# Optimization experiments

Measured on AMD Instinct MI355X. Metric: run time of the kernel, lower is better.

The kernel has to match this reference:

```python
import jax, jax.numpy as jnp
import numpy as np

N = 10000       # nodes
E = 160000      # edges
B = 100         # graphs
F_NODE = 32
F_EDGE = 16
H0, H1, H2, H3, H4, H5 = 32, 64, 128, 256, 128, 64
EPS = 1e-5


def setup_inputs() -> dict:
    key = jax.random.key(0)
    ks = jax.random.split(key, 32)

    def rn(k, shape):
        fan_in = shape[0] if len(shape) > 1 else shape[0]
        return jax.random.normal(k, shape, jnp.float32) / np.float32(np.sqrt(fan_in))

    inp = {}
    inp["x"] = jax.random.normal(ks[0], (N, F_NODE), jnp.float32)
    inp["edge_index"] = jax.random.randint(ks[1], (2, E), 0, N)
    inp["edge_attr"] = jax.random.normal(ks[2], (E, F_EDGE), jnp.float32)
    inp["batch"] = jnp.sort(jax.random.randint(ks[3], (N,), 0, B))
    # EdgeMLP: F_EDGE -> 128 -> 64 -> F_NODE*H0
    inp["We1"] = rn(ks[4], (F_EDGE, 128)); inp["be1"] = jnp.zeros((128,), jnp.float32)
    inp["We2"] = rn(ks[5], (128, 64));     inp["be2"] = jnp.zeros((64,), jnp.float32)
    inp["We3"] = rn(ks[6], (64, F_NODE * H0)); inp["be3"] = jnp.zeros((F_NODE * H0,), jnp.float32)
    # NNConv root linear + bias
    inp["Wroot"] = rn(ks[7], (F_NODE, H0)); inp["bc1"] = jnp.zeros((H0,), jnp.float32)
    # GATConv 1 (H0 -> H1, heads=1)
    inp["Wg1"] = rn(ks[8], (H0, H1)); inp["as1"] = rn(ks[9], (H1,)); inp["ad1"] = rn(ks[10], (H1,)); inp["bg1"] = jnp.zeros((H1,), jnp.float32)
    # GATConv 2 (H1 -> H2, heads=1)
    inp["Wg2"] = rn(ks[11], (H1, H2)); inp["as2"] = rn(ks[12], (H2,)); inp["ad2"] = rn(ks[13], (H2,)); inp["bg2"] = jnp.zeros((H2,), jnp.float32)
    # FC head
    inp["Wf1"] = rn(ks[14], (H2, H3)); inp["bf1"] = jnp.zeros((H3,), jnp.float32)
    inp["Wf2"] = rn(ks[15], (H3, H4)); inp["bf2"] = jnp.zeros((H4,), jnp.float32)
    inp["Wf3"] = rn(ks[16], (H4, H5)); inp["bf3"] = jnp.zeros((H5,), jnp.float32)
    return inp


def _bn(h):  # training-mode BatchNorm1d, affine = identity (default init)
    m = h.mean(axis=0)
    v = h.var(axis=0)
    return (h - m) * jax.lax.rsqrt(v + EPS)


def _seg_softmax(e, seg, n):
    m = jax.ops.segment_max(e, seg, num_segments=n)
    ex = jnp.exp(e - m[seg])
    s = jax.ops.segment_sum(ex, seg, num_segments=n)
    return ex / (s[seg] + 1e-16)


def _gat(x, src, dst, W, a_src, a_dst, b):
    n = x.shape[0]
    h = x @ W                                     # [N, F_out]
    loop = jnp.arange(n)                          # PyG add_self_loops=True
    s = jnp.concatenate([src, loop])
    d = jnp.concatenate([dst, loop])
    sc_s = h @ a_src                              # [N]
    sc_d = h @ a_dst
    e = jax.nn.leaky_relu(sc_s[s] + sc_d[d], negative_slope=0.2)
    alpha = _seg_softmax(e, d, n)                 # segment softmax over in-edges
    out = jax.ops.segment_sum(alpha[:, None] * h[s], d, num_segments=n)
    return out + b


def reference(x, edge_index, edge_attr, batch,
              We1, be1, We2, be2, We3, be3, Wroot, bc1,
              Wg1, as1, ad1, bg1, Wg2, as2, ad2, bg2,
              Wf1, bf1, Wf2, bf2, Wf3, bf3):
    src, dst = edge_index[0], edge_index[1]

    # --- NNConv: per-edge weight matrices from EdgeMLP ---
    t = jax.nn.relu(edge_attr @ We1 + be1)
    t = jax.nn.relu(t @ We2 + be2)
    theta = (t @ We3 + be3).reshape(E, F_NODE, H0)        # [E, F_in, F_out]
    msg = jnp.einsum('ef,efo->eo', x[src], theta)          # gather-matmul
    agg = jax.ops.segment_sum(msg, dst, num_segments=N)    # scatter-add (aggr='add')
    h = agg + x @ Wroot + bc1
    h = jax.nn.relu(_bn(h))

    # --- GATConv x2 ---
    h = jax.nn.relu(_bn(_gat(h, src, dst, Wg1, as1, ad1, bg1)))
    h = jax.nn.relu(_bn(_gat(h, src, dst, Wg2, as2, ad2, bg2)))

    # --- global mean pool ---
    sums = jax.ops.segment_sum(h, batch, num_segments=B)
    cnts = jax.ops.segment_sum(jnp.ones((N,), h.dtype), batch, num_segments=B)
    g = sums / jnp.maximum(cnts, 1.0)[:, None]             # [B, H2]

    # --- MLP head (dropout=Identity in eval/reference) ---
    g = jax.nn.relu(_bn(g @ Wf1 + bf1))
    g = jax.nn.relu(_bn(g @ Wf2 + bf2))
    return g @ Wf3 + bf3                                   # [B, H5]
```

## Files before the change

### kernel.cpp

```cpp
#include <hip/hip_runtime.h>

#define NN 10000
#define NE 160000
#define NGB 100

typedef __attribute__((ext_vector_type(8))) short s8v;
typedef __attribute__((ext_vector_type(4))) float f4v;
typedef __attribute__((ext_vector_type(2))) _Float16 h2v;
typedef __attribute__((ext_vector_type(8))) _Float16 h8v;

static __device__ __forceinline__ float lrelu(float v){ return v > 0.f ? v : 0.2f*v; }
static __device__ __forceinline__ unsigned short f2bf(float f){
  unsigned u = __float_as_uint(f);
  u += 0x7fffu + ((u >> 16) & 1u);
  return (unsigned short)(u >> 16);
}
static __device__ __forceinline__ float bf2f(unsigned short h){
  return __uint_as_float(((unsigned)h) << 16);
}
static __device__ __forceinline__ unsigned pkh(float a, float b){
  auto h = __builtin_amdgcn_cvt_pkrtz(a, b);
  return __builtin_bit_cast(unsigned, h);
}
static __device__ __forceinline__ unsigned short f2h(float f){
  _Float16 h = (_Float16)f;
  return __builtin_bit_cast(unsigned short, h);
}
static __device__ __forceinline__ float h2f(unsigned short u){
  return (float)__builtin_bit_cast(_Float16, u);
}

__global__ __launch_bounds__(256) void k_deg_bounds(const int* __restrict__ src, const int* __restrict__ dst,
                                                    const int* __restrict__ batch,
                                                    int* deg_src, int* deg_dst, int* starts){
  int i = blockIdx.x*256 + threadIdx.x;
  if (i < NE){ atomicAdd(&deg_src[src[i]],1); atomicAdd(&deg_dst[dst[i]],1); }
  if (i <= NN){
    int cur  = (i==NN) ? NGB : batch[i];
    int prev = (i==0)  ? -1  : batch[i-1];
    for (int b=prev+1; b<=cur; b++) if (b<=NGB) starts[b]=i;
  }
}

__global__ __launch_bounds__(1024) void k_scan(const int* __restrict__ deg_src, const int* __restrict__ deg_dst,
                                               int* rp_src, int* rp_dst){
  const int* deg = (blockIdx.x==0) ? deg_src : deg_dst;
  int* rp = (blockIdx.x==0) ? rp_src : rp_dst;
  __shared__ int part[1024];
  int tid = threadIdx.x;
  const int per = (NN + 1023)/1024;
  int base = tid*per;
  int s = 0;
  for (int i=0;i<per;i++){ int idx=base+i; if (idx<NN) s += deg[idx]; }
  part[tid]=s; __syncthreads();
  for (int off=1; off<1024; off<<=1){
    int v = part[tid];
    int add = (tid>=off) ? part[tid-off] : 0;
    __syncthreads();
    part[tid] = v + add;
    __syncthreads();
  }
  int run = (tid==0) ? 0 : part[tid-1];
  for (int i=0;i<per;i++){ int idx=base+i; if (idx<NN){ rp[idx]=run; run += deg[idx]; } }
  if (tid==1023) rp[NN] = part[1023];
}

__global__ __launch_bounds__(256) void k_fill(const int* __restrict__ src, const int* __restrict__ dst,
                       const int* __restrict__ rp_src, const int* __restrict__ rp_dst,
                       int* fill_src, int* fill_dst, int* pos_src, int* dstp, int* srcd, int* dstd){
  int i = blockIdx.x*256 + threadIdx.x;
  if (i < NE){
    int s=src[i], d=dst[i];
    int p=rp_src[s]+atomicAdd(&fill_src[s],1); pos_src[i]=p; dstp[p]=d;
    int q=rp_dst[d]+atomicAdd(&fill_dst[d],1); srcd[q]=s; dstd[q]=d;
  }
}

__global__ __launch_bounds__(256) void k_packall(const float* __restrict__ We1, const float* __restrict__ be1,
    const float* __restrict__ We2, const float* __restrict__ We3,
    unsigned short* __restrict__ W1p, unsigned short* __restrict__ W2p,
    unsigned short* __restrict__ W3h, unsigned short* __restrict__ W3l){
  int tid = threadIdx.x;
  if (blockIdx.x == 32){
    for (int idx=tid; idx<512; idx+=256){
      int j=idx>>6, l=idx&63, col=l&15, g=l>>4;
      int out = j*16+col;
      #pragma unroll
      for (int jj=0;jj<8;jj++){
        int k = g*8+jj;
        float v = (k<16) ? We1[k*128+out] : (k==16 ? be1[out] : 0.f);
        W1p[idx*8+jj] = f2bf(v);
      }
    }
    for (int idx=tid; idx<1024; idx+=256){
      int ft=idx>>6, l=idx&63, col=l&15, g=l>>4;
      int t=ft>>2, jo=ft&3;
      int out = jo*16+col;
      #pragma unroll
      for (int jj=0;jj<8;jj++){
        int k = t*32+g*8+jj;
        W2p[idx*8+jj] = f2bf(We2[k*64+out]);
      }
    }
  } else {
    int idx = blockIdx.x*256 + tid;
    int jt = idx>>6, l = idx&63;
    int j = jt*16 + (l&15);
    int f0 = (l>>4)*8;
    int k = j>>5, o = j&31;
    #pragma unroll
    for (int jj=0;jj<8;jj++){
      float v = We3[(size_t)k*1024 + (size_t)(f0+jj)*32 + o];
      unsigned short h = f2bf(v);
      float r = v - bf2f(h);
      W3h[(size_t)idx*8+jj] = h;
      W3l[(size_t)idx*8+jj] = f2bf(r);
    }
  }
}

__global__ __launch_bounds__(256) void k_edge_mlp2(const float* __restrict__ ea,
    const unsigned short* __restrict__ W1p, const unsigned short* __restrict__ W2p,
    const float* __restrict__ be2, const int* __restrict__ pos_src, unsigned* __restrict__ t2b){
  __shared__ unsigned short st1[4*2048];
  int tid=threadIdx.x, wave=tid>>6, lane=tid&63;
  int c = lane&15, g = lane>>4;
  s8v w1f[8], w2f[16];
  #pragma unroll
  for (int j=0;j<8;j++)  w1f[j] = *(const s8v*)(W1p + (size_t)(j*64+lane)*8);
  #pragma unroll
  for (int q=0;q<16;q++) w2f[q] = *(const s8v*)(W2p + (size_t)(q*64+lane)*8);
  float be2v[16];
  #pragma unroll
  for (int jo=0;jo<4;jo++)
    #pragma unroll
    for (int r=0;r<4;r++) be2v[jo*4+r] = be2[jo*16+g*4+r];
  char* myld = (char*)(st1 + wave*2048);
  const f4v fzero = {0.f,0.f,0.f,0.f};

  for (int base = blockIdx.x*64; base < NE; base += gridDim.x*64){
    int e0 = base + wave*16;
    s8v eaf = {0,0,0,0,0,0,0,0};
    if (g < 2){
      const float* p = ea + (size_t)(e0+c)*16 + g*8;
      float4 a = *(const float4*)p;
      float4 b = *(const float4*)(p+4);
      eaf[0]=(short)f2bf(a.x); eaf[1]=(short)f2bf(a.y); eaf[2]=(short)f2bf(a.z); eaf[3]=(short)f2bf(a.w);
      eaf[4]=(short)f2bf(b.x); eaf[5]=(short)f2bf(b.y); eaf[6]=(short)f2bf(b.z); eaf[7]=(short)f2bf(b.w);
    } else if (g == 2){
      eaf[0] = (short)0x3f80;
    }
    f4v acc1[8];
    #pragma unroll
    for (int j=0;j<8;j++)
      acc1[j] = __builtin_amdgcn_mfma_f32_16x16x32_bf16(w1f[j], eaf, fzero, 0, 0, 0);
    #pragma unroll
    for (int j=0;j<8;j++){
      unsigned lo = (unsigned)f2bf(fmaxf(acc1[j][0],0.f)) | ((unsigned)f2bf(fmaxf(acc1[j][1],0.f))<<16);
      unsigned hi = (unsigned)f2bf(fmaxf(acc1[j][2],0.f)) | ((unsigned)f2bf(fmaxf(acc1[j][3],0.f))<<16);
      unsigned off = (unsigned)(c*256 + ((j*32 + g*8) ^ (c<<4)));
      *(uint2*)(myld + off) = make_uint2(lo, hi);
    }
    __syncthreads();
    f4v acc2[4];
    #pragma unroll
    for (int jo=0;jo<4;jo++) acc2[jo] = fzero;
    #pragma unroll
    for (int t=0;t<4;t++){
      unsigned off = (unsigned)(c*256 + ((t*64 + g*16) ^ (c<<4)));
      s8v b2 = *(const s8v*)(myld + off);
      #pragma unroll
      for (int jo=0;jo<4;jo++)
        acc2[jo] = __builtin_amdgcn_mfma_f32_16x16x32_bf16(w2f[t*4+jo], b2, acc2[jo], 0, 0, 0);
    }
    int pos = pos_src[e0+c];
    unsigned* orow = t2b + (size_t)pos*32;
    #pragma unroll
    for (int jo=0;jo<4;jo++){
      float v0 = fmaxf(acc2[jo][0] + be2v[jo*4+0], 0.f);
      float v1 = fmaxf(acc2[jo][1] + be2v[jo*4+1], 0.f);
      float v2 = fmaxf(acc2[jo][2] + be2v[jo*4+2], 0.f);
      float v3 = fmaxf(acc2[jo][3] + be2v[jo*4+3], 0.f);
      *(uint2*)(orow + jo*8 + g*2) = make_uint2(pkh(v0,v1), pkh(v2,v3));
    }
    __syncthreads();
  }
}

__global__ __launch_bounds__(256) void k_y6(const float* __restrict__ x,
    const unsigned short* __restrict__ W3h, const unsigned short* __restrict__ W3l,
    unsigned* __restrict__ Yp){
  int tid=threadIdx.x, w=tid>>6, l=tid&63;
  int c = l&15, g = l>>4;
  int tile = blockIdx.x*2 + (w>>1);
  if (tile >= 625) return;
  int jhalf = w&1;
  int n = tile*16 + c;
  const float* xr = x + (size_t)n*32 + g*8;
  float4 xa = *(const float4*)xr;
  float4 xc = *(const float4*)(xr+4);
  float xv[8] = {xa.x,xa.y,xa.z,xa.w,xc.x,xc.y,xc.z,xc.w};
  s8v bh, bl;
  #pragma unroll
  for (int jj=0;jj<8;jj++){
    unsigned short h = f2bf(xv[jj]);
    bh[jj] = (short)h;
    bl[jj] = (short)f2bf(xv[jj] - bf2f(h));
  }
  const f4v fz = {0.f,0.f,0.f,0.f};
  unsigned* Yrow = Yp + (size_t)n*1024;
  for (int grp=0; grp<4; grp++){
    int jt_g0 = jhalf*64 + grp*16;
    int kpg = jhalf*4 + grp;
    uint4 Q[2][4];
    #pragma unroll
    for (int a=0; a<4; a++){
      #pragma unroll
      for (int b=0; b<2; b++){
        int jt_lo = jt_g0 + 4*a + b;
        int jt_hi = jt_lo + 2;
        s8v AhL = *(const s8v*)(W3h + (size_t)(jt_lo*64 + l)*8);
        s8v AlL = *(const s8v*)(W3l + (size_t)(jt_lo*64 + l)*8);
        f4v aL = __builtin_amdgcn_mfma_f32_16x16x32_bf16(AhL, bl, fz, 0, 0, 0);
        aL = __builtin_amdgcn_mfma_f32_16x16x32_bf16(AlL, bh, aL, 0, 0, 0);
        aL = __builtin_amdgcn_mfma_f32_16x16x32_bf16(AhL, bh, aL, 0, 0, 0);
        s8v AhH = *(const s8v*)(W3h + (size_t)(jt_hi*64 + l)*8);
        s8v AlH = *(const s8v*)(W3l + (size_t)(jt_hi*64 + l)*8);
        f4v aH = __builtin_amdgcn_mfma_f32_16x16x32_bf16(AhH, bl, fz, 0, 0, 0);
        aH = __builtin_amdgcn_mfma_f32_16x16x32_bf16(AlH, bh, aH, 0, 0, 0);
        aH = __builtin_amdgcn_mfma_f32_16x16x32_bf16(AhH, bh, aH, 0, 0, 0);
        #pragma unroll
        for (int r=0;r<4;r++){
          unsigned pv = pkh(aL[r], aH[r]);
          if (a==0) Q[b][r].x = pv;
          else if (a==1) Q[b][r].y = pv;
          else if (a==2) Q[b][r].z = pv;
          else Q[b][r].w = pv;
        }
      }
    }
    #pragma unroll
    for (int b=0;b<2;b++)
      #pragma unroll
      for (int r=0;r<4;r++){
        int o = b*16 + g*4 + r;
        *(uint4*)(Yrow + kpg*128 + o*4) = Q[b][r];
      }
  }
}

__global__ __launch_bounds__(256) void k_xbagg(const float* __restrict__ x,
    const float* __restrict__ be3, const float* __restrict__ Wroot, const float* __restrict__ bc1,
    float* __restrict__ xb, float* __restrict__ agg){
  __shared__ __align__(16) float sx[8][32];
  int oo = threadIdx.x & 31, nn = threadIdx.x >> 5;
  float wb[32], wr[32];
  #pragma unroll
  for (int f=0;f<32;f++){ wb[f]=be3[f*32+oo]; wr[f]=Wroot[f*32+oo]; }
  float bcv = bc1[oo];
  int per = (1250 + gridDim.x - 1)/gridDim.x;
  int g0 = blockIdx.x*per, g1 = min(g0+per, 1250);
  for (int gi=g0; gi<g1; gi++){
    int nb = gi*8;
    __syncthreads();
    sx[threadIdx.x>>5][threadIdx.x&31] = x[(size_t)nb*32 + threadIdx.x];
    __syncthreads();
    float a1=0.f, a2=0.f;
    #pragma unroll
    for (int f4=0;f4<8;f4++){
      float4 xvv = *(const float4*)(&sx[nn][f4*4]);
      a1 += xvv.x*wb[f4*4+0]+xvv.y*wb[f4*4+1]+xvv.z*wb[f4*4+2]+xvv.w*wb[f4*4+3];
      a2 += xvv.x*wr[f4*4+0]+xvv.y*wr[f4*4+1]+xvv.z*wr[f4*4+2]+xvv.w*wr[f4*4+3];
    }
    xb[(size_t)(nb+nn)*32+oo] = a1;
    agg[(size_t)(nb+nn)*32+oo] = a2 + bcv;
  }
}

__global__ __launch_bounds__(256) void k_msg4(const unsigned* __restrict__ Yp,
    const float* __restrict__ xb, const unsigned* __restrict__ t2b,
    const int* __restrict__ rp_src, const int* __restrict__ dstp,
    float* __restrict__ agg){
  int tid=threadIdx.x, w=tid>>6, lane=tid&63;
  int c = lane&15, g = lane>>4;
  int gw = blockIdx.x*4 + w, stride = gridDim.x*4;
  const f4v fz = {0.f,0.f,0.f,0.f};
  for (int n=gw; n<NN; n+=stride){
    int beg=rp_src[n], end=rp_src[n+1];
    if (beg==end) continue;
    const unsigned* Yr = Yp + (size_t)n*1024;
    h8v B[2][2];
    #pragma unroll
    for (int kt=0;kt<2;kt++)
      #pragma unroll
      for (int jn=0;jn<2;jn++)
        B[kt][jn] = __builtin_bit_cast(h8v, *(const uint4*)(Yr + (kt*4+g)*128 + (jn*16+c)*4));
    float xq0 = xb[(size_t)n*32 + c];
    float xq1 = xb[(size_t)n*32 + c + 16];
    for (int eb=beg; eb<end; eb+=16){
      const unsigned* tr = t2b + (size_t)(eb + c)*32;
      h8v A0 = __builtin_bit_cast(h8v, *(const uint4*)(tr + g*4));
      h8v A1 = __builtin_bit_cast(h8v, *(const uint4*)(tr + 16 + g*4));
      f4v acc0 = __builtin_amdgcn_mfma_f32_16x16x32_f16(A0, B[0][0], fz, 0, 0, 0);
      acc0 = __builtin_amdgcn_mfma_f32_16x16x32_f16(A1, B[1][0], acc0, 0, 0, 0);
      f4v acc1 = __builtin_amdgcn_mfma_f32_16x16x32_f16(A0, B[0][1], fz, 0, 0, 0);
      acc1 = __builtin_amdgcn_mfma_f32_16x16x32_f16(A1, B[1][1], acc1, 0, 0, 0);
      #pragma unroll
      for (int r=0;r<4;r++){
        int p = eb + g*4 + r;
        if (p < end){
          int d = dstp[p];
          float* ap = agg + (size_t)d*32;
          unsafeAtomicAdd(ap + c,      acc0[r] + xq0);
          unsafeAtomicAdd(ap + c + 16, acc1[r] + xq1);
        }
      }
    }
  }
}

__global__ __launch_bounds__(256) void k_stats(const float* __restrict__ buf, int nrows, int ncols,
                                               float* __restrict__ stats){
  int tid = threadIdx.x;
  int c  = tid % ncols;
  int r0 = tid / ncols;
  int rp = 256 / ncols;
  float s1=0.f, s2=0.f;
  for (long long base=(long long)blockIdx.x*rp; base<nrows; base+=(long long)gridDim.x*rp){
    int r = (int)base + r0;
    if (r < nrows){
      float v = buf[(size_t)r*ncols + c];
      s1 += v; s2 += v*v;
    }
  }
  __shared__ float A[256], B[256];
  A[tid]=s1; B[tid]=s2; __syncthreads();
  if (tid < ncols){
    float t1=0.f, t2=0.f;
    for (int gg=0; gg<256/ncols; gg++){ t1 += A[gg*ncols+tid]; t2 += B[gg*ncols+tid]; }
    atomicAdd(&stats[tid], t1);
    atomicAdd(&stats[ncols+tid], t2);
  }
}

template<int FIN, int FOUT>
__global__ __launch_bounds__(256) void k_gat_linear(const float* __restrict__ raw,
    const float* __restrict__ stats, const float* __restrict__ W,
    const float* __restrict__ avs, const float* __restrict__ avd,
    unsigned short* __restrict__ hWh, float* __restrict__ sc_s, float* __restrict__ sc_d){
  __shared__ float sW[FIN*FOUT];
  __shared__ float sA[FOUT], sD[FOUT];
  __shared__ float sScale[FIN], sShift[FIN];
  __shared__ float sIn[4][FIN];
  int tid = threadIdx.x;
  for (int i=tid;i<FIN*FOUT;i+=256) sW[i]=W[i];
  if (tid<FOUT){ sA[tid]=avs[tid]; sD[tid]=avd[tid]; }
  if (tid<FIN){
    float m = stats[tid]*(1.f/NN);
    float v = stats[FIN+tid]*(1.f/NN) - m*m;
    float s = rsqrtf(v + 1e-5f);
    sScale[tid]=s; sShift[tid]=-m*s;
  }
  __syncthreads();
  int wave=tid>>6, lane=tid&63;
  for (int nb = blockIdx.x*4; nb < NN; nb += gridDim.x*4){
    int n = nb + wave;
    bool act = n < NN;
    if (act){
      for (int ff=lane; ff<FIN; ff+=64){
        float vv = raw[(size_t)n*FIN+ff]*sScale[ff]+sShift[ff];
        sIn[wave][ff] = fmaxf(vv, 0.f);
      }
    }
    __syncthreads();
    if (act){
      float out0=0.f, out1=0.f;
      #pragma unroll
      for (int ff=0; ff<FIN; ff++){
        float xv = sIn[wave][ff];
        out0 += xv*sW[ff*FOUT+lane];
        if constexpr (FOUT > 64) out1 += xv*sW[ff*FOUT+lane+64];
      }
      hWh[(size_t)n*FOUT + lane] = f2h(out0);
      float ps = out0*sA[lane], pd = out0*sD[lane];
      if constexpr (FOUT > 64){
        hWh[(size_t)n*FOUT + lane + 64] = f2h(out1);
        ps += out1*sA[lane+64]; pd += out1*sD[lane+64];
      }
      #pragma unroll
      for (int off=32;off>0;off>>=1){ ps += __shfl_down(ps,off); pd += __shfl_down(pd,off); }
      if (lane==0){ sc_s[n]=ps; sc_d[n]=pd; }
    }
    __syncthreads();
  }
}

__global__ __launch_bounds__(256) void k_escore(const float* __restrict__ sc_s, const float* __restrict__ sc_d,
    const int* __restrict__ srcd, const int* __restrict__ dstd, float* __restrict__ sce){
  int q = blockIdx.x*256 + threadIdx.x;
  if (q < NE) sce[q] = lrelu(sc_s[srcd[q]] + sc_d[dstd[q]]);
}

template<int F>
__global__ __launch_bounds__(256) void k_gat_attn4(const unsigned short* __restrict__ hWh,
    const float* __restrict__ sce, const float* __restrict__ sc_s, const float* __restrict__ sc_d,
    const int* __restrict__ rp_dst, const int* __restrict__ srcd,
    const float* __restrict__ bias, float* __restrict__ outraw){
  int tid=threadIdx.x, w=tid>>6, lane=tid&63;
  int gw = blockIdx.x*4 + w, stride = gridDim.x*4;
  for (int n=gw; n<NN; n+=stride){
    int beg=rp_dst[n], end=rp_dst[n+1];
    float M=-3e38f, S=0.f, acc0=0.f, acc1=0.f;
    for (int base=beg; base<end; base+=64){
      int nb = min(64, end-base);
      float sc=-3e38f; int si=0;
      if (lane<nb){ sc = sce[base+lane]; si = srcd[base+lane]; }
      float cm=sc;
      #pragma unroll
      for (int off=32;off>0;off>>=1) cm = fmaxf(cm, __shfl_xor(cm,off));
      float Mn = fmaxf(M, cm);
      float p = (lane<nb) ? __expf(sc-Mn) : 0.f;
      float ps=p;
      #pragma unroll
      for (int off=32;off>0;off>>=1) ps += __shfl_xor(ps,off);
      float scale = __expf(M-Mn);
      S = S*scale + ps;
      acc0*=scale; acc1*=scale;
      int jj=0;
      for (; jj+4<=nb; jj+=4){
        float p0=__shfl(p,jj), p1=__shfl(p,jj+1), p2=__shfl(p,jj+2), p3=__shfl(p,jj+3);
        int   q0=__shfl(si,jj), q1=__shfl(si,jj+1), q2=__shfl(si,jj+2), q3=__shfl(si,jj+3);
        if constexpr (F==128){
          unsigned u0 = *(const unsigned*)(hWh + (size_t)q0*128 + 2*lane);
          unsigned u1 = *(const unsigned*)(hWh + (size_t)q1*128 + 2*lane);
          unsigned u2 = *(const unsigned*)(hWh + (size_t)q2*128 + 2*lane);
          unsigned u3 = *(const unsigned*)(hWh + (size_t)q3*128 + 2*lane);
          acc0 += p0*h2f((unsigned short)(u0&0xffffu)); acc1 += p0*h2f((unsigned short)(u0>>16));
          acc0 += p1*h2f((unsigned short)(u1&0xffffu)); acc1 += p1*h2f((unsigned short)(u1>>16));
          acc0 += p2*h2f((unsigned short)(u2&0xffffu)); acc1 += p2*h2f((unsigned short)(u2>>16));
          acc0 += p3*h2f((unsigned short)(u3&0xffffu)); acc1 += p3*h2f((unsigned short)(u3>>16));
        } else {
          float v0 = h2f(hWh[(size_t)q0*64+lane]);
          float v1 = h2f(hWh[(size_t)q1*64+lane]);
          float v2 = h2f(hWh[(size_t)q2*64+lane]);
          float v3 = h2f(hWh[(size_t)q3*64+lane]);
          acc0 += p0*v0 + p1*v1 + p2*v2 + p3*v3;
        }
      }
      for (; jj<nb; jj++){
        float pj=__shfl(p,jj); int qj=__shfl(si,jj);
        if constexpr (F==128){
          unsigned u = *(const unsigned*)(hWh + (size_t)qj*128 + 2*lane);
          acc0 += pj*h2f((unsigned short)(u&0xffffu));
          acc1 += pj*h2f((unsigned short)(u>>16));
        } else {
          acc0 += pj*h2f(hWh[(size_t)qj*64+lane]);
        }
      }
      M = Mn;
    }
    float sself = lrelu(sc_s[n]+sc_d[n]);
    float Mn = fmaxf(M, sself);
    float scale = __expf(M-Mn);
    float pself = __expf(sself-Mn);
    S = S*scale + pself;
    acc0*=scale; acc1*=scale;
    float inv = 1.f/(S+1e-16f);
    if constexpr (F==128){
      unsigned u = *(const unsigned*)(hWh + (size_t)n*128 + 2*lane);
      acc0 += pself*h2f((unsigned short)(u&0xffffu));
      acc1 += pself*h2f((unsigned short)(u>>16));
      float ox = acc0*inv + bias[2*lane];
      float oy = acc1*inv + bias[2*lane+1];
      *(float2*)(outraw + (size_t)n*128 + 2*lane) = make_float2(ox, oy);
    } else {
      acc0 += pself*h2f(hWh[(size_t)n*64+lane]);
      outraw[(size_t)n*64+lane] = acc0*inv + bias[lane];
    }
  }
}

__global__ __launch_bounds__(256) void k_pool(const float* __restrict__ h2raw,
    const float* __restrict__ stats, const int* __restrict__ starts,
    float* __restrict__ g){
  __shared__ float sc[128], sh[128];
  __shared__ float red[256];
  int b=blockIdx.x, t=threadIdx.x;
  if (t<128){
    float m = stats[t]*(1.f/NN);
    float v = stats[128+t]*(1.f/NN) - m*m;
    float s = rsqrtf(v+1e-5f);
    sc[t]=s; sh[t]=-m*s;
  }
  __syncthreads();
  int s0=starts[b], s1=starts[b+1];
  int f=t&127, half=t>>7;
  float acc=0.f;
  for (int n=s0+half;n<s1;n+=2){
    float v = h2raw[(size_t)n*128+f]*sc[f]+sh[f];
    acc += fmaxf(v,0.f);
  }
  red[t]=acc; __syncthreads();
  if (half==0){
    int cnt = s1-s0;
    g[b*128+f] = (red[f]+red[128+f]) / fmaxf((float)cnt, 1.f);
  }
}

__global__ __launch_bounds__(256) void k_head1(const float* __restrict__ g,
    const float* __restrict__ Wf1, const float* __restrict__ bf1, float* __restrict__ g1,
    float* __restrict__ statsH1){
  __shared__ float sg[128];
  int r=blockIdx.x, t=threadIdx.x;
  if (t<128) sg[t]=g[r*128+t];
  __syncthreads();
  float acc=bf1[t];
  #pragma unroll 4
  for (int k=0;k<128;k++) acc += sg[k]*Wf1[k*256+t];
  g1[r*256+t]=acc;
  atomicAdd(&statsH1[t], acc);
  atomicAdd(&statsH1[256+t], acc*acc);
}

__global__ __launch_bounds__(256) void k_head2(const float* __restrict__ g1,
    const float* __restrict__ stats, const float* __restrict__ Wf2,
    const float* __restrict__ bf2, float* __restrict__ g2, float* __restrict__ statsH2){
  __shared__ float sin_[256];
  int r=blockIdx.x, t=threadIdx.x;
  float m = stats[t]*(1.f/NGB);
  float v = stats[256+t]*(1.f/NGB) - m*m;
  float val = (g1[r*256+t]-m)*rsqrtf(v+1e-5f);
  sin_[t]=fmaxf(val,0.f);
  __syncthreads();
  if (t<128){
    float acc=bf2[t];
    #pragma unroll 4
    for (int k=0;k<256;k++) acc += sin_[k]*Wf2[k*128+t];
    g2[r*128+t]=acc;
    atomicAdd(&statsH2[t], acc);
    atomicAdd(&statsH2[128+t], acc*acc);
  }
}

__global__ __launch_bounds__(256) void k_head3(const float* __restrict__ g2,
    const float* __restrict__ stats, const float* __restrict__ Wf3,
    const float* __restrict__ bf3, float* __restrict__ out){
  __shared__ float sin_[128];
  int r=blockIdx.x, t=threadIdx.x;
  if (t<128){
    float m = stats[t]*(1.f/NGB);
    float v = stats[128+t]*(1.f/NGB) - m*m;
    float val = (g2[r*128+t]-m)*rsqrtf(v+1e-5f);
    sin_[t]=fmaxf(val,0.f);
  }
  __syncthreads();
  if (t<64){
    float acc=bf3[t];
    #pragma unroll 4
    for (int k=0;k<128;k++) acc += sin_[k]*Wf3[k*64+t];
    out[r*64+t]=acc;
  }
}

extern "C" void kernel_launch(void* const* d_in, const int* in_sizes, int n_in,
                              void* d_out, int out_size, void* d_ws, size_t ws_size,
                              hipStream_t stream){
  const float* x    = (const float*)d_in[0];
  const int*   ei   = (const int*)d_in[1];
  const float* ea   = (const float*)d_in[2];
  const int*   batch= (const int*)d_in[3];
  const float* We1=(const float*)d_in[4];  const float* be1=(const float*)d_in[5];
  const float* We2=(const float*)d_in[6];  const float* be2=(const float*)d_in[7];
  const float* We3=(const float*)d_in[8];  const float* be3=(const float*)d_in[9];
  const float* Wroot=(const float*)d_in[10]; const float* bc1=(const float*)d_in[11];
  const float* Wg1=(const float*)d_in[12]; const float* as1=(const float*)d_in[13];
  const float* ad1=(const float*)d_in[14]; const float* bg1=(const float*)d_in[15];
  const float* Wg2=(const float*)d_in[16]; const float* as2=(const float*)d_in[17];
  const float* ad2=(const float*)d_in[18]; const float* bg2=(const float*)d_in[19];
  const float* Wf1=(const float*)d_in[20]; const float* bf1=(const float*)d_in[21];
  const float* Wf2=(const float*)d_in[22]; const float* bf2=(const float*)d_in[23];
  const float* Wf3=(const float*)d_in[24]; const float* bf3=(const float*)d_in[25];
  (void)in_sizes; (void)n_in; (void)out_size; (void)ws_size;
  float* out = (float*)d_out;
  char* ws = (char*)d_ws;
  const int* srcA = ei;
  const int* dstA = ei + NE;

  size_t off = 0;
  auto take = [&](size_t bytes)->size_t{ size_t r = off; off += (bytes + 255) & ~(size_t)255; return r; };
  size_t o_deg_src = take(NN*4), o_deg_dst = take(NN*4);
  size_t o_fill_src = take(NN*4), o_fill_dst = take(NN*4);
  size_t o_stats0 = take(2*32*4), o_stats1 = take(2*64*4), o_stats2 = take(2*128*4);
  size_t o_statsH1 = take(2*256*4), o_statsH2 = take(2*128*4);
  size_t zero_bytes = off;
  size_t o_rp_src = take((NN+1)*4), o_rp_dst = take((NN+1)*4);
  size_t o_pos_src = take((size_t)NE*4);
  size_t o_dstp = take((size_t)NE*4);
  size_t o_srcd = take((size_t)NE*4);
  size_t o_dstd = take((size_t)NE*4);
  size_t o_sce  = take((size_t)NE*4);
  size_t o_starts = take((NGB+1)*4);
  size_t o_W1p = take(4096*2);
  size_t o_W2p = take(8192*2);
  size_t o_W3h = take((size_t)128*64*8*2);
  size_t o_W3l = take((size_t)128*64*8*2);
  size_t o_t2b = take((size_t)(NE+16)*32*4);
  size_t o_Yp  = take((size_t)NN*1024*4);
  size_t o_xb  = take((size_t)NN*32*4);
  size_t o_agg = take((size_t)NN*32*4);
  size_t o_hW1 = take((size_t)NN*64*2);
  size_t o_scs1 = take(NN*4), o_scd1 = take(NN*4);
  size_t o_h1  = take((size_t)NN*64*4);
  size_t o_hW2 = take((size_t)NN*128*2);
  size_t o_scs2 = take(NN*4), o_scd2 = take(NN*4);
  size_t o_h2  = take((size_t)NN*128*4);
  size_t o_g   = take(NGB*128*4);
  size_t o_g1  = take(NGB*256*4);
  size_t o_g2  = take(NGB*128*4);

  #define WF(o) ((float*)(ws + (o)))
  #define WI(o) ((int*)(ws + (o)))
  #define WU(o) ((unsigned short*)(ws + (o)))
  #define WW(o) ((unsigned*)(ws + (o)))

  (void)hipMemsetAsync(ws, 0, zero_bytes, stream);
  k_deg_bounds<<<625,256,0,stream>>>(srcA,dstA,batch,WI(o_deg_src),WI(o_deg_dst),WI(o_starts));
  k_scan<<<2,1024,0,stream>>>(WI(o_deg_src),WI(o_deg_dst),WI(o_rp_src),WI(o_rp_dst));
  k_fill<<<625,256,0,stream>>>(srcA,dstA,WI(o_rp_src),WI(o_rp_dst),
                               WI(o_fill_src),WI(o_fill_dst),
                               WI(o_pos_src),WI(o_dstp),WI(o_srcd),WI(o_dstd));
  k_packall<<<33,256,0,stream>>>(We1,be1,We2,We3,WU(o_W1p),WU(o_W2p),WU(o_W3h),WU(o_W3l));
  k_edge_mlp2<<<500,256,0,stream>>>(ea,WU(o_W1p),WU(o_W2p),be2,WI(o_pos_src),WW(o_t2b));
  k_y6<<<313,256,0,stream>>>(x,WU(o_W3h),WU(o_W3l),WW(o_Yp));
  k_xbagg<<<256,256,0,stream>>>(x,be3,Wroot,bc1,WF(o_xb),WF(o_agg));
  k_msg4<<<2500,256,0,stream>>>(WW(o_Yp),WF(o_xb),WW(o_t2b),WI(o_rp_src),WI(o_dstp),WF(o_agg));

  k_stats<<<64,256,0,stream>>>(WF(o_agg),NN,32,WF(o_stats0));
  k_gat_linear<32,64><<<640,256,0,stream>>>(WF(o_agg),WF(o_stats0),Wg1,as1,ad1,
                                            WU(o_hW1),WF(o_scs1),WF(o_scd1));
  k_escore<<<625,256,0,stream>>>(WF(o_scs1),WF(o_scd1),WI(o_srcd),WI(o_dstd),WF(o_sce));
  k_gat_attn4<64><<<2500,256,0,stream>>>(WU(o_hW1),WF(o_sce),WF(o_scs1),WF(o_scd1),
                                         WI(o_rp_dst),WI(o_srcd),bg1,WF(o_h1));
  k_stats<<<64,256,0,stream>>>(WF(o_h1),NN,64,WF(o_stats1));
  k_gat_linear<64,128><<<640,256,0,stream>>>(WF(o_h1),WF(o_stats1),Wg2,as2,ad2,
                                             WU(o_hW2),WF(o_scs2),WF(o_scd2));
  k_escore<<<625,256,0,stream>>>(WF(o_scs2),WF(o_scd2),WI(o_srcd),WI(o_dstd),WF(o_sce));
  k_gat_attn4<128><<<2500,256,0,stream>>>(WU(o_hW2),WF(o_sce),WF(o_scs2),WF(o_scd2),
                                          WI(o_rp_dst),WI(o_srcd),bg2,WF(o_h2));
  k_stats<<<64,256,0,stream>>>(WF(o_h2),NN,128,WF(o_stats2));

  k_pool<<<NGB,256,0,stream>>>(WF(o_h2),WF(o_stats2),WI(o_starts),WF(o_g));
  k_head1<<<NGB,256,0,stream>>>(WF(o_g),Wf1,bf1,WF(o_g1),WF(o_statsH1));
  k_head2<<<NGB,256,0,stream>>>(WF(o_g1),WF(o_statsH1),Wf2,bf2,WF(o_g2),WF(o_statsH2));
  k_head3<<<NGB,256,0,stream>>>(WF(o_g2),WF(o_statsH2),Wf3,bf3,out);
}
```

Baseline: 288.4 us.

## Merge independent prep, edge-MLP, Y and root kernels into fewer launches

Folds the weight-packing kernel into the degree/bounds kernel, merges the edge MLP, the per-node Y precompute and the xb/agg root linear into one block-partitioned kernel, and fuses mean pooling with the first head layer. The aim is to cut launch overhead and let independent stages run side by side on the GPU. In exchange the fused kernel shares one register/LDS budget across its branches, which may lower occupancy for the lighter branches. The edge-MLP grid-stride count also changes from 500 to 625 blocks.

```diff
diff --git a/kernel.cpp b/kernel.cpp
--- a/kernel.cpp
+++ b/kernel.cpp
@@ -30,15 +30,56 @@
   return (float)__builtin_bit_cast(_Float16, u);
 }
 
-__global__ __launch_bounds__(256) void k_deg_bounds(const int* __restrict__ src, const int* __restrict__ dst,
-                                                    const int* __restrict__ batch,
-                                                    int* deg_src, int* deg_dst, int* starts){
+__global__ __launch_bounds__(256) void k_prep(const int* __restrict__ src, const int* __restrict__ dst,
+    const int* __restrict__ batch,
+    const float* __restrict__ We1, const float* __restrict__ be1,
+    const float* __restrict__ We2, const float* __restrict__ We3,
+    int* deg_src, int* deg_dst, int* starts,
+    unsigned short* __restrict__ W1p, unsigned short* __restrict__ W2p,
+    unsigned short* __restrict__ W3h, unsigned short* __restrict__ W3l){
   int i = blockIdx.x*256 + threadIdx.x;
   if (i < NE){ atomicAdd(&deg_src[src[i]],1); atomicAdd(&deg_dst[dst[i]],1); }
   if (i <= NN){
     int cur  = (i==NN) ? NGB : batch[i];
     int prev = (i==0)  ? -1  : batch[i-1];
     for (int b=prev+1; b<=cur; b++) if (b<=NGB) starts[b]=i;
+  }
+  int tid = threadIdx.x;
+  if (blockIdx.x == 32){
+    for (int idx=tid; idx<512; idx+=256){
+      int j=idx>>6, l=idx&63, col=l&15, g=l>>4;
+      int out = j*16+col;
+      #pragma unroll
+      for (int jj=0;jj<8;jj++){
+        int k = g*8+jj;
+        float v = (k<16) ? We1[k*128+out] : (k==16 ? be1[out] : 0.f);
+        W1p[idx*8+jj] = f2bf(v);
+      }
+    }
+    for (int idx=tid; idx<1024; idx+=256){
+      int ft=idx>>6, l=idx&63, col=l&15, g=l>>4;
+      int t=ft>>2, jo=ft&3;
+      int out = jo*16+col;
+      #pragma unroll
+      for (int jj=0;jj<8;jj++){
+        int k = t*32+g*8+jj;
+        W2p[idx*8+jj] = f2bf(We2[k*64+out]);
+      }
+    }
+  } else if (blockIdx.x < 32){
+    int idx = blockIdx.x*256 + tid;
+    int jt = idx>>6, l = idx&63;
+    int j = jt*16 + (l&15);
+    int f0 = (l>>4)*8;
+    int k = j>>5, o = j&31;
+    #pragma unroll
+    for (int jj=0;jj<8;jj++){
+      float v = We3[(size_t)k*1024 + (size_t)(f0+jj)*32 + o];
+      unsigned short h = f2bf(v);
+      float r = v - bf2f(h);
+      W3h[(size_t)idx*8+jj] = h;
+      W3l[(size_t)idx*8+jj] = f2bf(r);
+    }
   }
 }
 
@@ -76,204 +117,159 @@
   }
 }
 
-__global__ __launch_bounds__(256) void k_packall(const float* __restrict__ We1, const float* __restrict__ be1,
-    const float* __restrict__ We2, const float* __restrict__ We3,
-    unsigned short* __restrict__ W1p, unsigned short* __restrict__ W2p,
-    unsigned short* __restrict__ W3h, unsigned short* __restrict__ W3l){
-  int tid = threadIdx.x;
-  if (blockIdx.x == 32){
-    for (int idx=tid; idx<512; idx+=256){
-      int j=idx>>6, l=idx&63, col=l&15, g=l>>4;
-      int out = j*16+col;
-      #pragma unroll
-      for (int jj=0;jj<8;jj++){
-        int k = g*8+jj;
-        float v = (k<16) ? We1[k*128+out] : (k==16 ? be1[out] : 0.f);
-        W1p[idx*8+jj] = f2bf(v);
-      }
-    }
-    for (int idx=tid; idx<1024; idx+=256){
-      int ft=idx>>6, l=idx&63, col=l&15, g=l>>4;
-      int t=ft>>2, jo=ft&3;
-      int out = jo*16+col;
-      #pragma unroll
-      for (int jj=0;jj<8;jj++){
-        int k = t*32+g*8+jj;
-        W2p[idx*8+jj] = f2bf(We2[k*64+out]);
-      }
-    }
-  } else {
-    int idx = blockIdx.x*256 + tid;
-    int jt = idx>>6, l = idx&63;
-    int j = jt*16 + (l&15);
-    int f0 = (l>>4)*8;
-    int k = j>>5, o = j&31;
+__global__ __launch_bounds__(256) void k_big(const float* __restrict__ ea,
+    const unsigned short* __restrict__ W1p, const unsigned short* __restrict__ W2p,
+    const float* __restrict__ be2, const int* __restrict__ pos_src, unsigned* __restrict__ t2b,
+    const float* __restrict__ x,
+    const unsigned short* __restrict__ W3h, const unsigned short* __restrict__ W3l,
+    unsigned* __restrict__ Yp,
+    const float* __restrict__ be3, const float* __restrict__ Wroot, const float* __restrict__ bc1,
+    float* __restrict__ xb, float* __restrict__ agg){
+  __shared__ unsigned short st1[4*2048];
+  int bid = blockIdx.x;
+  int tid=threadIdx.x, wave=tid>>6, lane=tid&63;
+  const f4v fz = {0.f,0.f,0.f,0.f};
+  if (bid < 625){
+    int c = lane&15, g = lane>>4;
+    s8v w1f[8], w2f[16];
+    #pragma unroll
+    for (int j=0;j<8;j++)  w1f[j] = *(const s8v*)(W1p + (size_t)(j*64+lane)*8);
+    #pragma unroll
+    for (int q=0;q<16;q++) w2f[q] = *(const s8v*)(W2p + (size_t)(q*64+lane)*8);
+    float be2v[16];
+    #pragma unroll
+    for (int jo=0;jo<4;jo++)
+      #pragma unroll
+      for (int r=0;r<4;r++) be2v[jo*4+r] = be2[jo*16+g*4+r];
+    char* myld = (char*)(st1 + wave*2048);
+    for (int base = bid*64; base < NE; base += 625*64){
+      int e0 = base + wave*16;
+      s8v eaf = {0,0,0,0,0,0,0,0};
+      if (g < 2){
+        const float* p = ea + (size_t)(e0+c)*16 + g*8;
+        float4 a = *(const float4*)p;
+        float4 b = *(const float4*)(p+4);
+        eaf[0]=(short)f2bf(a.x); eaf[1]=(short)f2bf(a.y); eaf[2]=(short)f2bf(a.z); eaf[3]=(short)f2bf(a.w);
+        eaf[4]=(short)f2bf(b.x); eaf[5]=(short)f2bf(b.y); eaf[6]=(short)f2bf(b.z); eaf[7]=(short)f2bf(b.w);
+      } else if (g == 2){
+        eaf[0] = (short)0x3f80;
+      }
+      f4v acc1[8];
+      #pragma unroll
+      for (int j=0;j<8;j++)
+        acc1[j] = __builtin_amdgcn_mfma_f32_16x16x32_bf16(w1f[j], eaf, fz, 0, 0, 0);
+      #pragma unroll
+      for (int j=0;j<8;j++){
+        unsigned lo = (unsigned)f2bf(fmaxf(acc1[j][0],0.f)) | ((unsigned)f2bf(fmaxf(acc1[j][1],0.f))<<16);
+        unsigned hi = (unsigned)f2bf(fmaxf(acc1[j][2],0.f)) | ((unsigned)f2bf(fmaxf(acc1[j][3],0.f))<<16);
+        unsigned off = (unsigned)(c*256 + ((j*32 + g*8) ^ (c<<4)));
+        *(uint2*)(myld + off) = make_uint2(lo, hi);
+      }
+      __syncthreads();
+      f4v acc2[4];
+      #pragma unroll
+      for (int jo=0;jo<4;jo++) acc2[jo] = fz;
+      #pragma unroll
+      for (int t=0;t<4;t++){
+        unsigned off = (unsigned)(c*256 + ((t*64 + g*16) ^ (c<<4)));
+        s8v b2 = *(const s8v*)(myld + off);
+        #pragma unroll
+        for (int jo=0;jo<4;jo++)
+          acc2[jo] = __builtin_amdgcn_mfma_f32_16x16x32_bf16(w2f[t*4+jo], b2, acc2[jo], 0, 0, 0);
+      }
+      int pos = pos_src[e0+c];
+      unsigned* orow = t2b + (size_t)pos*32;
+      #pragma unroll
+      for (int jo=0;jo<4;jo++){
+        float v0 = fmaxf(acc2[jo][0] + be2v[jo*4+0], 0.f);
+        float v1 = fmaxf(acc2[jo][1] + be2v[jo*4+1], 0.f);
+        float v2 = fmaxf(acc2[jo][2] + be2v[jo*4+2], 0.f);
+        float v3 = fmaxf(acc2[jo][3] + be2v[jo*4+3], 0.f);
+        *(uint2*)(orow + jo*8 + g*2) = make_uint2(pkh(v0,v1), pkh(v2,v3));
+      }
+      __syncthreads();
+    }
+  } else if (bid < 938){
+    int c = lane&15, g = lane>>4;
+    int tile = (bid-625)*2 + (wave>>1);
+    if (tile >= 625) return;
+    int jhalf = wave&1;
+    int n = tile*16 + c;
+    const float* xr = x + (size_t)n*32 + g*8;
+    float4 xa = *(const float4*)xr;
+    float4 xc = *(const float4*)(xr+4);
+    float xv[8] = {xa.x,xa.y,xa.z,xa.w,xc.x,xc.y,xc.z,xc.w};
+    s8v bh, bl;
     #pragma unroll
     for (int jj=0;jj<8;jj++){
-      float v = We3[(size_t)k*1024 + (size_t)(f0+jj)*32 + o];
-      unsigned short h = f2bf(v);
-      float r = v - bf2f(h);
-      W3h[(size_t)idx*8+jj] = h;
-      W3l[(size_t)idx*8+jj] = f2bf(r);
-    }
-  }
-}
-
-__global__ __launch_bounds__(256) void k_edge_mlp2(const float* __restrict__ ea,
-    const unsigned short* __restrict__ W1p, const unsigned short* __restrict__ W2p,
-    const float* __restrict__ be2, const int* __restrict__ pos_src, unsigned* __restrict__ t2b){
-  __shared__ unsigned short st1[4*2048];
-  int tid=threadIdx.x, wave=tid>>6, lane=tid&63;
-  int c = lane&15, g = lane>>4;
-  s8v w1f[8], w2f[16];
-  #pragma unroll
-  for (int j=0;j<8;j++)  w1f[j] = *(const s8v*)(W1p + (size_t)(j*64+lane)*8);
-  #pragma unroll
-  for (int q=0;q<16;q++) w2f[q] = *(const s8v*)(W2p + (size_t)(q*64+lane)*8);
-  float be2v[16];
-  #pragma unroll
-  for (int jo=0;jo<4;jo++)
-    #pragma unroll
-    for (int r=0;r<4;r++) be2v[jo*4+r] = be2[jo*16+g*4+r];
-  char* myld = (char*)(st1 + wave*2048);
-  const f4v fzero = {0.f,0.f,0.f,0.f};
-
-  for (int base = blockIdx.x*64; base < NE; base += gridDim.x*64){
-    int e0 = base + wave*16;
-    s8v eaf = {0,0,0,0,0,0,0,0};
-    if (g < 2){
-      const float* p = ea + (size_t)(e0+c)*16 + g*8;
-      float4 a = *(const float4*)p;
-      float4 b = *(const float4*)(p+4);
-      eaf[0]=(short)f2bf(a.x); eaf[1]=(short)f2bf(a.y); eaf[2]=(short)f2bf(a.z); eaf[3]=(short)f2bf(a.w);
-      eaf[4]=(short)f2bf(b.x); eaf[5]=(short)f2bf(b.y); eaf[6]=(short)f2bf(b.z); eaf[7]=(short)f2bf(b.w);
-    } else if (g == 2){
-      eaf[0] = (short)0x3f80;
-    }
-    f4v acc1[8];
-    #pragma unroll
-    for (int j=0;j<8;j++)
-      acc1[j] = __builtin_amdgcn_mfma_f32_16x16x32_bf16(w1f[j], eaf, fzero, 0, 0, 0);
-    #pragma unroll
-    for (int j=0;j<8;j++){
-      unsigned lo = (unsigned)f2bf(fmaxf(acc1[j][0],0.f)) | ((unsigned)f2bf(fmaxf(acc1[j][1],0.f))<<16);
-      unsigned hi = (unsigned)f2bf(fmaxf(acc1[j][2],0.f)) | ((unsigned)f2bf(fmaxf(acc1[j][3],0.f))<<16);
-      unsigned off = (unsigned)(c*256 + ((j*32 + g*8) ^ (c<<4)));
-      *(uint2*)(myld + off) = make_uint2(lo, hi);
-    }
-    __syncthreads();
-    f4v acc2[4];
-    #pragma unroll
-    for (int jo=0;jo<4;jo++) acc2[jo] = fzero;
-    #pragma unroll
-    for (int t=0;t<4;t++){
-      unsigned off = (unsigned)(c*256 + ((t*64 + g*16) ^ (c<<4)));
-      s8v b2 = *(const s8v*)(myld + off);
-      #pragma unroll
-      for (int jo=0;jo<4;jo++)
-        acc2[jo] = __builtin_amdgcn_mfma_f32_16x16x32_bf16(w2f[t*4+jo], b2, acc2[jo], 0, 0, 0);
-    }
-    int pos = pos_src[e0+c];
-    unsigned* orow = t2b + (size_t)pos*32;
-    #pragma unroll
-    for (int jo=0;jo<4;jo++){
-      float v0 = fmaxf(acc2[jo][0] + be2v[jo*4+0], 0.f);
-      float v1 = fmaxf(acc2[jo][1] + be2v[jo*4+1], 0.f);
-      float v2 = fmaxf(acc2[jo][2] + be2v[jo*4+2], 0.f);
-      float v3 = fmaxf(acc2[jo][3] + be2v[jo*4+3], 0.f);
-      *(uint2*)(orow + jo*8 + g*2) = make_uint2(pkh(v0,v1), pkh(v2,v3));
-    }
-    __syncthreads();
-  }
-}
-
-__global__ __launch_bounds__(256) void k_y6(const float* __restrict__ x,
-    const unsigned short* __restrict__ W3h, const unsigned short* __restrict__ W3l,
-    unsigned* __restrict__ Yp){
-  int tid=threadIdx.x, w=tid>>6, l=tid&63;
-  int c = l&15, g = l>>4;
-  int tile = blockIdx.x*2 + (w>>1);
-  if (tile >= 625) return;
-  int jhalf = w&1;
-  int n = tile*16 + c;
-  const float* xr = x + (size_t)n*32 + g*8;
-  float4 xa = *(const float4*)xr;
-  float4 xc = *(const float4*)(xr+4);
-  float xv[8] = {xa.x,xa.y,xa.z,xa.w,xc.x,xc.y,xc.z,xc.w};
-  s8v bh, bl;
-  #pragma unroll
-  for (int jj=0;jj<8;jj++){
-    unsigned short h = f2bf(xv[jj]);
-    bh[jj] = (short)h;
-    bl[jj] = (short)f2bf(xv[jj] - bf2f(h));
-  }
-  const f4v fz = {0.f,0.f,0.f,0.f};
-  unsigned* Yrow = Yp + (size_t)n*1024;
-  for (int grp=0; grp<4; grp++){
-    int jt_g0 = jhalf*64 + grp*16;
-    int kpg = jhalf*4 + grp;
-    uint4 Q[2][4];
-    #pragma unroll
-    for (int a=0; a<4; a++){
-      #pragma unroll
-      for (int b=0; b<2; b++){
-        int jt_lo = jt_g0 + 4*a + b;
-        int jt_hi = jt_lo + 2;
-        s8v AhL = *(const s8v*)(W3h + (size_t)(jt_lo*64 + l)*8);
-        s8v AlL = *(const s8v*)(W3l + (size_t)(jt_lo*64 + l)*8);
-        f4v aL = __builtin_amdgcn_mfma_f32_16x16x32_bf16(AhL, bl, fz, 0, 0, 0);
-        aL = __builtin_amdgcn_mfma_f32_16x16x32_bf16(AlL, bh, aL, 0, 0, 0);
-        aL = __builtin_amdgcn_mfma_f32_16x16x32_bf16(AhL, bh, aL, 0, 0, 0);
-        s8v AhH = *(const s8v*)(W3h + (size_t)(jt_hi*64 + l)*8);
-        s8v AlH = *(const s8v*)(W3l + (size_t)(jt_hi*64 + l)*8);
-        f4v aH = __builtin_amdgcn_mfma_f32_16x16x32_bf16(AhH, bl, fz, 0, 0, 0);
-        aH = __builtin_amdgcn_mfma_f32_16x16x32_bf16(AlH, bh, aH, 0, 0, 0);
-        aH = __builtin_amdgcn_mfma_f32_16x16x32_bf16(AhH, bh, aH, 0, 0, 0);
+      unsigned short h = f2bf(xv[jj]);
+      bh[jj] = (short)h;
+      bl[jj] = (short)f2bf(xv[jj] - bf2f(h));
+    }
+    unsigned* Yrow = Yp + (size_t)n*1024;
+    for (int grp=0; grp<4; grp++){
+      int jt_g0 = jhalf*64 + grp*16;
+      int kpg = jhalf*4 + grp;
+      uint4 Q[2][4];
+      #pragma unroll
+      for (int a=0; a<4; a++){
+        #pragma unroll
+        for (int b=0; b<2; b++){
+          int jt_lo = jt_g0 + 4*a + b;
+          int jt_hi = jt_lo + 2;
+          s8v AhL = *(const s8v*)(W3h + (size_t)(jt_lo*64 + lane)*8);
+          s8v AlL = *(const s8v*)(W3l + (size_t)(jt_lo*64 + lane)*8);
+          f4v aL = __builtin_amdgcn_mfma_f32_16x16x32_bf16(AhL, bl, fz, 0, 0, 0);
+          aL = __builtin_amdgcn_mfma_f32_16x16x32_bf16(AlL, bh, aL, 0, 0, 0);
+          aL = __builtin_amdgcn_mfma_f32_16x16x32_bf16(AhL, bh, aL, 0, 0, 0);
+          s8v AhH = *(const s8v*)(W3h + (size_t)(jt_hi*64 + lane)*8);
+          s8v AlH = *(const s8v*)(W3l + (size_t)(jt_hi*64 + lane)*8);
+          f4v aH = __builtin_amdgcn_mfma_f32_16x16x32_bf16(AhH, bl, fz, 0, 0, 0);
+          aH = __builtin_amdgcn_mfma_f32_16x16x32_bf16(AlH, bh, aH, 0, 0, 0);
+          aH = __builtin_amdgcn_mfma_f32_16x16x32_bf16(AhH, bh, aH, 0, 0, 0);
+          #pragma unroll
+          for (int r=0;r<4;r++){
+            unsigned pv = pkh(aL[r], aH[r]);
+            if (a==0) Q[b][r].x = pv;
+            else if (a==1) Q[b][r].y = pv;
+            else if (a==2) Q[b][r].z = pv;
+            else Q[b][r].w = pv;
+          }
+        }
+      }
+      #pragma unroll
+      for (int b=0;b<2;b++)
         #pragma unroll
         for (int r=0;r<4;r++){
-          unsigned pv = pkh(aL[r], aH[r]);
-          if (a==0) Q[b][r].x = pv;
-          else if (a==1) Q[b][r].y = pv;
-          else if (a==2) Q[b][r].z = pv;
-          else Q[b][r].w = pv;
+          int o = b*16 + g*4 + r;
+          *(uint4*)(Yrow + kpg*128 + o*4) = Q[b][r];
         }
-      }
-    }
+    }
+  } else {
+    __shared__ __align__(16) float sx[8][32];
+    int b2 = bid - 938;
+    int oo = tid & 31, nn = tid >> 5;
+    float wb[32], wr[32];
     #pragma unroll
-    for (int b=0;b<2;b++)
-      #pragma unroll
-      for (int r=0;r<4;r++){
-        int o = b*16 + g*4 + r;
-        *(uint4*)(Yrow + kpg*128 + o*4) = Q[b][r];
-      }
-  }
-}
-
-__global__ __launch_bounds__(256) void k_xbagg(const float* __restrict__ x,
-    const float* __restrict__ be3, const float* __restrict__ Wroot, const float* __restrict__ bc1,
-    float* __restrict__ xb, float* __restrict__ agg){
-  __shared__ __align__(16) float sx[8][32];
-  int oo = threadIdx.x & 31, nn = threadIdx.x >> 5;
-  float wb[32], wr[32];
-  #pragma unroll
-  for (int f=0;f<32;f++){ wb[f]=be3[f*32+oo]; wr[f]=Wroot[f*32+oo]; }
-  float bcv = bc1[oo];
-  int per = (1250 + gridDim.x - 1)/gridDim.x;
-  int g0 = blockIdx.x*per, g1 = min(g0+per, 1250);
-  for (int gi=g0; gi<g1; gi++){
-    int nb = gi*8;
-    __syncthreads();
-    sx[threadIdx.x>>5][threadIdx.x&31] = x[(size_t)nb*32 + threadIdx.x];
-    __syncthreads();
-    float a1=0.f, a2=0.f;
-    #pragma unroll
-    for (int f4=0;f4<8;f4++){
-      float4 xvv = *(const float4*)(&sx[nn][f4*4]);
-      a1 += xvv.x*wb[f4*4+0]+xvv.y*wb[f4*4+1]+xvv.z*wb[f4*4+2]+xvv.w*wb[f4*4+3];
-      a2 += xvv.x*wr[f4*4+0]+xvv.y*wr[f4*4+1]+xvv.z*wr[f4*4+2]+xvv.w*wr[f4*4+3];
-    }
-    xb[(size_t)(nb+nn)*32+oo] = a1;
-    agg[(size_t)(nb+nn)*32+oo] = a2 + bcv;
+    for (int f=0;f<32;f++){ wb[f]=be3[f*32+oo]; wr[f]=Wroot[f*32+oo]; }
+    float bcv = bc1[oo];
+    int per = (1250 + 63)/64;
+    int g0 = b2*per, g1 = min(g0+per, 1250);
+    for (int gi=g0; gi<g1; gi++){
+      int nb = gi*8;
+      __syncthreads();
+      sx[tid>>5][tid&31] = x[(size_t)nb*32 + tid];
+      __syncthreads();
+      float a1=0.f, a2=0.f;
+      #pragma unroll
+      for (int f4=0;f4<8;f4++){
+        float4 xvv = *(const float4*)(&sx[nn][f4*4]);
+        a1 += xvv.x*wb[f4*4+0]+xvv.y*wb[f4*4+1]+xvv.z*wb[f4*4+2]+xvv.w*wb[f4*4+3];
+        a2 += xvv.x*wr[f4*4+0]+xvv.y*wr[f4*4+1]+xvv.z*wr[f4*4+2]+xvv.w*wr[f4*4+3];
+      }
+      xb[(size_t)(nb+nn)*32+oo] = a1;
+      agg[(size_t)(nb+nn)*32+oo] = a2 + bcv;
+    }
   }
 }
 
@@ -480,11 +476,11 @@
   }
 }
 
-__global__ __launch_bounds__(256) void k_pool(const float* __restrict__ h2raw,
+__global__ __launch_bounds__(256) void k_poolhead1(const float* __restrict__ h2raw,
     const float* __restrict__ stats, const int* __restrict__ starts,
-    float* __restrict__ g){
-  __shared__ float sc[128], sh[128];
-  __shared__ float red[256];
+    const float* __restrict__ Wf1, const float* __restrict__ bf1,
+    float* __restrict__ g1, float* __restrict__ statsH1){
+  __shared__ float sc[128], sh[128], red[256], sg[128];
   int b=blockIdx.x, t=threadIdx.x;
   if (t<128){
     float m = stats[t]*(1.f/NN);
@@ -503,23 +499,15 @@
   red[t]=acc; __syncthreads();
   if (half==0){
     int cnt = s1-s0;
-    g[b*128+f] = (red[f]+red[128+f]) / fmaxf((float)cnt, 1.f);
-  }
-}
-
-__global__ __launch_bounds__(256) void k_head1(const float* __restrict__ g,
-    const float* __restrict__ Wf1, const float* __restrict__ bf1, float* __restrict__ g1,
-    float* __restrict__ statsH1){
-  __shared__ float sg[128];
-  int r=blockIdx.x, t=threadIdx.x;
-  if (t<128) sg[t]=g[r*128+t];
+    sg[f] = (red[f]+red[128+f]) / fmaxf((float)cnt, 1.f);
+  }
   __syncthreads();
-  float acc=bf1[t];
+  float a = bf1[t];
   #pragma unroll 4
-  for (int k=0;k<128;k++) acc += sg[k]*Wf1[k*256+t];
-  g1[r*256+t]=acc;
-  atomicAdd(&statsH1[t], acc);
-  atomicAdd(&statsH1[256+t], acc*acc);
+  for (int k=0;k<128;k++) a += sg[k]*Wf1[k*256+t];
+  g1[b*256+t]=a;
+  atomicAdd(&statsH1[t], a);
+  atomicAdd(&statsH1[256+t], a*a);
 }
 
 __global__ __launch_bounds__(256) void k_head2(const float* __restrict__ g1,
@@ -614,7 +602,6 @@
   size_t o_hW2 = take((size_t)NN*128*2);
   size_t o_scs2 = take(NN*4), o_scd2 = take(NN*4);
   size_t o_h2  = take((size_t)NN*128*4);
-  size_t o_g   = take(NGB*128*4);
   size_t o_g1  = take(NGB*256*4);
   size_t o_g2  = take(NGB*128*4);
 
@@ -624,15 +611,16 @@
   #define WW(o) ((unsigned*)(ws + (o)))
 
   (void)hipMemsetAsync(ws, 0, zero_bytes, stream);
-  k_deg_bounds<<<625,256,0,stream>>>(srcA,dstA,batch,WI(o_deg_src),WI(o_deg_dst),WI(o_starts));
+  k_prep<<<625,256,0,stream>>>(srcA,dstA,batch,We1,be1,We2,We3,
+                               WI(o_deg_src),WI(o_deg_dst),WI(o_starts),
+                               WU(o_W1p),WU(o_W2p),WU(o_W3h),WU(o_W3l));
   k_scan<<<2,1024,0,stream>>>(WI(o_deg_src),WI(o_deg_dst),WI(o_rp_src),WI(o_rp_dst));
   k_fill<<<625,256,0,stream>>>(srcA,dstA,WI(o_rp_src),WI(o_rp_dst),
                                WI(o_fill_src),WI(o_fill_dst),
                                WI(o_pos_src),WI(o_dstp),WI(o_srcd),WI(o_dstd));
-  k_packall<<<33,256,0,stream>>>(We1,be1,We2,We3,WU(o_W1p),WU(o_W2p),WU(o_W3h),WU(o_W3l));
-  k_edge_mlp2<<<500,256,0,stream>>>(ea,WU(o_W1p),WU(o_W2p),be2,WI(o_pos_src),WW(o_t2b));
-  k_y6<<<313,256,0,stream>>>(x,WU(o_W3h),WU(o_W3l),WW(o_Yp));
-  k_xbagg<<<256,256,0,stream>>>(x,be3,Wroot,bc1,WF(o_xb),WF(o_agg));
+  k_big<<<1002,256,0,stream>>>(ea,WU(o_W1p),WU(o_W2p),be2,WI(o_pos_src),WW(o_t2b),
+                               x,WU(o_W3h),WU(o_W3l),WW(o_Yp),
+                               be3,Wroot,bc1,WF(o_xb),WF(o_agg));
   k_msg4<<<2500,256,0,stream>>>(WW(o_Yp),WF(o_xb),WW(o_t2b),WI(o_rp_src),WI(o_dstp),WF(o_agg));
 
   k_stats<<<64,256,0,stream>>>(WF(o_agg),NN,32,WF(o_stats0));
@@ -649,8 +637,8 @@
                                           WI(o_rp_dst),WI(o_srcd),bg2,WF(o_h2));
   k_stats<<<64,256,0,stream>>>(WF(o_h2),NN,128,WF(o_stats2));
 
-  k_pool<<<NGB,256,0,stream>>>(WF(o_h2),WF(o_stats2),WI(o_starts),WF(o_g));
-  k_head1<<<NGB,256,0,stream>>>(WF(o_g),Wf1,bf1,WF(o_g1),WF(o_statsH1));
+  k_poolhead1<<<NGB,256,0,stream>>>(WF(o_h2),WF(o_stats2),WI(o_starts),Wf1,bf1,
+                                    WF(o_g1),WF(o_statsH1));
   k_head2<<<NGB,256,0,stream>>>(WF(o_g1),WF(o_statsH1),Wf2,bf2,WF(o_g2),WF(o_statsH2));
   k_head3<<<NGB,256,0,stream>>>(WF(o_g2),WF(o_statsH2),Wf3,bf3,out);
 }
```

Result: faster. 266.3 us (-7.7%).
